# Kernel tuning notes

Hardware: AMD Instinct MI355X
Metric: run time of the kernel (lower is better)

Reference implementation:

```python
import jax, jax.numpy as jnp
import numpy as np

E = 1024
H = 16
HD = E // H  # head_dim = 64
N, T, S = 2, 2048, 2048
NEG = -1e9


def setup_inputs() -> dict:
    key = jax.random.key(0)
    ks = jax.random.split(key, 12)
    s = 0.02
    inp = {
        "query": jax.random.normal(ks[0], (N, T, E), jnp.float32),
        "key": jax.random.normal(ks[1], (N, S, E), jnp.float32),
        "value": jax.random.normal(ks[2], (N, S, E), jnp.float32),
        # causal mask: mask[i, j] == 0 means target i cannot attend to source j
        "attn_mask": jnp.tril(jnp.ones((T, S), jnp.float32)),
        "pad_mask": jnp.zeros((N, S), bool),
        "Wq": jax.random.normal(ks[3], (E, E), jnp.float32) * s,
        "bq": jnp.zeros((E,), jnp.float32),
        "Wk": jax.random.normal(ks[4], (E, E), jnp.float32) * s,
        "bk": jnp.zeros((E,), jnp.float32),
        "Wv": jax.random.normal(ks[5], (E, E), jnp.float32) * s,
        "bv": jnp.zeros((E,), jnp.float32),
        "Wp": jax.random.normal(ks[6], (E, E), jnp.float32) * s,
        "bp": jnp.zeros((E,), jnp.float32),
    }
    return inp


def reference(query, key, value, attn_mask, pad_mask, Wq, bq, Wk, bk, Wv, bv, Wp, bp):
    n, t, _ = query.shape
    _, srcl, _ = key.shape
    # Linear projections (torch Linear: x @ W.T + b), split into heads
    Q = (query @ Wq.T + bq).reshape(n, t, H, HD).transpose(0, 2, 1, 3)      # (N,H,T,HD)
    K = (key @ Wk.T + bk).reshape(n, srcl, H, HD).transpose(0, 2, 1, 3)     # (N,H,S,HD)
    V = (value @ Wv.T + bv).reshape(n, srcl, H, HD).transpose(0, 2, 1, 3)   # (N,H,S,HD)
    scores = jnp.einsum("nhtd,nhsd->nhts", Q, K) / jnp.sqrt(jnp.float32(HD))
    scores = jnp.where(pad_mask[:, None, None, :], NEG, scores)
    scores = jnp.where(attn_mask[None, None, :, :] == 0, NEG, scores)
    att = jax.nn.softmax(scores, axis=-1)  # dropout=0 (eval)
    Y = jnp.einsum("nhts,nhsd->nhtd", att, V)
    Y = Y.transpose(0, 2, 1, 3).reshape(n, t, E)
    return Y @ Wp.T + bp
```

## Files before the change

kernel.cpp:

```cpp
#include <hip/hip_runtime.h>
#include <hip/hip_bf16.h>

#define E_  1024
#define H_  16
#define HD_ 64
#define NB  2
#define T_  2048
#define S_  2048
#define KD  1024

#define QSCALE 0.18033688011112042f

typedef __attribute__((ext_vector_type(8))) short short8;
typedef __attribute__((ext_vector_type(4))) short short4v;
typedef __attribute__((ext_vector_type(4))) float floatx4;

static __device__ __forceinline__ unsigned short f2bf(float f) {
    unsigned int u = __float_as_uint(f);
    unsigned int r = (u + 0x7FFFu + ((u >> 16) & 1u)) >> 16;
    return (unsigned short)r;
}

static __device__ __forceinline__ unsigned short f2bf_fast(float f) {
    return (unsigned short)((__float_as_uint(f) + 0x8000u) >> 16);
}

static __device__ __forceinline__ floatx4 mfma16(short8 a, short8 b, floatx4 c) {
    return __builtin_amdgcn_mfma_f32_16x16x32_bf16(a, b, c, 0, 0, 0);
}

static __device__ __forceinline__ void gload_lds16(const void* g, void* l) {
    __builtin_amdgcn_global_load_lds(
        (const __attribute__((address_space(1))) unsigned int*)g,
        (__attribute__((address_space(3))) unsigned int*)l, 16, 0, 0);
}

#define VMCNT0_BARRIER() do {                                   \
    __builtin_amdgcn_sched_barrier(0);                          \
    asm volatile("s_waitcnt vmcnt(0)" ::: "memory");            \
    __builtin_amdgcn_s_barrier();                               \
    __builtin_amdgcn_sched_barrier(0);                          \
} while (0)

__global__ __launch_bounds__(256) void conv_all_kernel(
    const float* __restrict__ wq, const float* __restrict__ wk,
    const float* __restrict__ wv, const float* __restrict__ wp,
    const float* __restrict__ qi, const float* __restrict__ ki,
    const float* __restrict__ vi,
    unsigned short* __restrict__ Wb, unsigned short* __restrict__ Xb)
{
    const int NW4 = 1 << 18;
    const int NX4 = 1 << 20;
    const int TOT = 4 * NW4 + 3 * NX4;
    int idx = blockIdx.x * 256 + threadIdx.x;
    for (int i4 = idx; i4 < TOT; i4 += 262144) {
        const float* s; unsigned short* d; int off4;
        float sc = 1.0f;
        if (i4 < 4 * NW4) {
            int seg = i4 >> 18; off4 = i4 & (NW4 - 1);
            s = (seg == 0) ? wq : (seg == 1) ? wk : (seg == 2) ? wv : wp;
            d = Wb + ((size_t)seg << 20);
            if (seg == 0) sc = QSCALE;
        } else {
            int j = i4 - 4 * NW4; int seg = j >> 20; off4 = j & (NX4 - 1);
            s = (seg == 0) ? qi : (seg == 1) ? ki : vi;
            d = Xb + ((size_t)seg << 22);
        }
        float4 v = *(const float4*)&s[(size_t)off4 * 4];
        short4v b;
        b[0] = (short)f2bf(v.x * sc); b[1] = (short)f2bf(v.y * sc);
        b[2] = (short)f2bf(v.z * sc); b[3] = (short)f2bf(v.w * sc);
        *(short4v*)&d[(size_t)off4 * 4] = b;
    }
}

__global__ __launch_bounds__(256) void proj_qkv_kernel(
    const unsigned short* __restrict__ Xb, const unsigned short* __restrict__ Wb,
    const float* __restrict__ bq, const float* __restrict__ bk, const float* __restrict__ bv,
    unsigned short* __restrict__ Qh, unsigned short* __restrict__ K2, unsigned short* __restrict__ V2)
{
    const int z = blockIdx.z;
    const unsigned short* X = Xb + ((size_t)z << 22);
    const unsigned short* W = Wb + ((size_t)z << 20);
    const float* bias = (z == 0) ? bq : (z == 1) ? bk : bv;
    unsigned short* dst = (z == 0) ? Qh : (z == 1) ? K2 : V2;

    __shared__ unsigned short Sm[32768];

    const int tid  = threadIdx.x;
    const int lane = tid & 63;
    const int w    = tid >> 6;
    const int wm   = w >> 1, wn = w & 1;
    const int m0   = blockIdx.x * 128;
    const int e0   = blockIdx.y * 128;
    const int l15  = lane & 15, lg = lane >> 4;

    floatx4 acc[4][4];
#pragma unroll
    for (int mi = 0; mi < 4; ++mi)
#pragma unroll
        for (int ni = 0; ni < 4; ++ni)
            acc[mi][ni] = (floatx4){0.f, 0.f, 0.f, 0.f};

    const int rc = lane >> 3;
    const int sl = (lane & 7) ^ rc;

#pragma unroll
    for (int jj = 0; jj < 4; ++jj) {
        int c = w * 4 + jj;
        int row = c * 8 + rc;
        gload_lds16(&X[(size_t)(m0 + row) * KD + sl * 8], &Sm[c * 512]);
        gload_lds16(&W[(size_t)(e0 + row) * KD + sl * 8], &Sm[16384 + c * 512]);
    }
    VMCNT0_BARRIER();

    for (int kt = 0; kt < 16; ++kt) {
        const int cur = (kt & 1) * 8192;
        const int nxt = ((kt + 1) & 1) * 8192;
        const unsigned short* Ac = Sm + cur;
        const unsigned short* Bc = Sm + 16384 + cur;
        unsigned short* An = Sm + nxt;
        unsigned short* Bn = Sm + 16384 + nxt;
        const int k0n = (kt + 1) * 64;

        if (kt < 15) {
#pragma unroll
            for (int jj = 0; jj < 4; ++jj) {
                int c = w * 4 + jj;
                int row = c * 8 + rc;
                gload_lds16(&X[(size_t)(m0 + row) * KD + k0n + sl * 8], &An[c * 512]);
            }
        }
        {
            short8 af[4], bf[4];
#pragma unroll
            for (int mi = 0; mi < 4; ++mi) {
                int r_ = wm * 64 + mi * 16 + l15;
                af[mi] = *(const short8*)&Ac[r_ * 64 + ((lg ^ (r_ & 7)) << 3)];
            }
#pragma unroll
            for (int ni = 0; ni < 4; ++ni) {
                int r_ = wn * 64 + ni * 16 + l15;
                bf[ni] = *(const short8*)&Bc[r_ * 64 + ((lg ^ (r_ & 7)) << 3)];
            }
#pragma unroll
            for (int mi = 0; mi < 4; ++mi)
#pragma unroll
                for (int ni = 0; ni < 4; ++ni)
                    acc[mi][ni] = mfma16(af[mi], bf[ni], acc[mi][ni]);
        }
        if (kt < 15) {
#pragma unroll
            for (int jj = 0; jj < 4; ++jj) {
                int c = w * 4 + jj;
                int row = c * 8 + rc;
                gload_lds16(&W[(size_t)(e0 + row) * KD + k0n + sl * 8], &Bn[c * 512]);
            }
        }
        {
            short8 af[4], bf[4];
#pragma unroll
            for (int mi = 0; mi < 4; ++mi) {
                int r_ = wm * 64 + mi * 16 + l15;
                af[mi] = *(const short8*)&Ac[r_ * 64 + (((4 + lg) ^ (r_ & 7)) << 3)];
            }
#pragma unroll
            for (int ni = 0; ni < 4; ++ni) {
                int r_ = wn * 64 + ni * 16 + l15;
                bf[ni] = *(const short8*)&Bc[r_ * 64 + (((4 + lg) ^ (r_ & 7)) << 3)];
            }
#pragma unroll
            for (int mi = 0; mi < 4; ++mi)
#pragma unroll
                for (int ni = 0; ni < 4; ++ni)
                    acc[mi][ni] = mfma16(af[mi], bf[ni], acc[mi][ni]);
        }
        VMCNT0_BARRIER();
    }

    if (z != 2) {
#pragma unroll
        for (int mi = 0; mi < 4; ++mi)
#pragma unroll
            for (int ni = 0; ni < 4; ++ni) {
                int col = wn * 64 + ni * 16 + l15;
                float bb = bias[e0 + col];
                if (z == 0) bb *= QSCALE;
#pragma unroll
                for (int r = 0; r < 4; ++r) {
                    int row = wm * 64 + mi * 16 + (lg << 2) + r;
                    Sm[row * 128 + (col ^ ((row & 7) << 3))] =
                        f2bf(acc[mi][ni][r] + bb);
                }
            }
    } else {
#pragma unroll
        for (int mi = 0; mi < 4; ++mi)
#pragma unroll
            for (int ni = 0; ni < 4; ++ni) {
                int col = wn * 64 + ni * 16 + l15;
                float bb = bias[e0 + col];
                int rb = wm * 64 + mi * 16 + (lg << 2);
                short4v sv;
#pragma unroll
                for (int r = 0; r < 4; ++r) sv[r] = (short)f2bf(acc[mi][ni][r] + bb);
                *(short4v*)&Sm[col * 128 + (rb ^ ((col & 7) << 3))] = sv;
            }
    }
    __syncthreads();

    {
        const int r0 = tid >> 1;
        const int cb = (tid & 1) * 64;
#pragma unroll
        for (int j = 0; j < 8; ++j) {
            int c = cb + j * 8;
            short8 v = *(const short8*)&Sm[r0 * 128 + (c ^ ((r0 & 7) << 3))];
            if (z == 0) {
                int m = m0 + r0, nn = m >> 11, t = m & (T_ - 1);
                int e = e0 + c, hh = e >> 6, d = e & 63;
                size_t hb = (size_t)(nn * H_ + hh) * (T_ * HD_);
                *(short8*)&dst[hb + (size_t)t * HD_ + d] = v;
            } else if (z == 1) {
                int m = m0 + r0, nn = m >> 11, t = m & (T_ - 1);
                int e = e0 + c, hh = e >> 6, d = e & 63;
                size_t hb = (size_t)(nn * H_ + hh) * (T_ * HD_);
                *(short8*)&dst[hb + (t >> 6) * 4096 + (t & 63) * 64 +
                               (((d >> 3) ^ (t & 7)) << 3)] = v;
            } else {
                int e = e0 + r0, hh = e >> 6, d = e & 63;
                int m = m0 + c, nn = m >> 11, t = m & (T_ - 1);
                size_t hb = (size_t)(nn * H_ + hh) * (T_ * HD_);
                *(short8*)&dst[hb + (t >> 6) * 4096 + d * 64 +
                               ((((t >> 3) & 7) ^ (d & 7)) << 3)] = v;
            }
        }
    }
}

__global__ __launch_bounds__(256) void flash_attn_kernel(
    const unsigned short* __restrict__ Qh, const unsigned short* __restrict__ K2,
    const unsigned short* __restrict__ V2, unsigned short* __restrict__ Y)
{
    const int linear = blockIdx.x;
    const int nid = (linear & 7) * 64 + (linear >> 3);
    const int pb = nid & 15, h = (nid >> 4) & 15, n = nid >> 8;

    const int tid = threadIdx.x, lane = tid & 63, w = tid >> 6;
    const int l15 = lane & 15, lg = lane >> 4;

    const unsigned short* Qp = Qh + (size_t)(n * H_ + h) * (T_ * HD_);
    const unsigned short* Kt = K2 + (size_t)(n * H_ + h) * (T_ * HD_);
    const unsigned short* Vt = V2 + (size_t)(n * H_ + h) * (T_ * HD_);

    __shared__ unsigned short Ks_l[8192];
    __shared__ unsigned short VT_l[8192];
    __shared__ unsigned short Ps[64][136];

    const int prow = w * 16 + lg * 4;
    const int arow = w * 16 + l15;
    const int sw7  = l15 & 7;

#pragma unroll
    for (int side = 0; side < 2; ++side) {
        const int qt = side ? (31 - pb) : pb;
        const int q0 = qt * 64;
        const int nkv = (qt + 2) >> 1;

        short8 qf[2];
#pragma unroll
        for (int ks = 0; ks < 2; ++ks)
            qf[ks] = *(const short8*)&Qp[(size_t)(q0 + arow) * HD_ + ks * 32 + lg * 8];

        floatx4 o[4];
        float lacc[4];
#pragma unroll
        for (int hi = 0; hi < 4; ++hi) o[hi] = (floatx4){0.f, 0.f, 0.f, 0.f};
#pragma unroll
        for (int r = 0; r < 4; ++r) lacc[r] = 0.f;

        for (int kb2 = 0; kb2 < nkv; ++kb2) {
            __syncthreads();
            const unsigned short* Ksrc = Kt + kb2 * 8192;
            const unsigned short* Vsrc = Vt + kb2 * 8192;
#pragma unroll
            for (int j = 0; j < 4; ++j) {
                int c = w * 4 + j;
                gload_lds16(&Ksrc[c * 512 + lane * 8], &Ks_l[c * 512]);
                gload_lds16(&Vsrc[c * 512 + lane * 8], &VT_l[c * 512]);
            }
            __syncthreads();

            floatx4 sa[8];
#pragma unroll
            for (int ni = 0; ni < 8; ++ni) sa[ni] = (floatx4){0.f, 0.f, 0.f, 0.f};
            __builtin_amdgcn_s_setprio(1);
#pragma unroll
            for (int ks = 0; ks < 2; ++ks) {
                short8 kf[8];
#pragma unroll
                for (int ni = 0; ni < 8; ++ni)
                    kf[ni] = *(const short8*)
                        &Ks_l[(ni * 16 + l15) * 64 + (((ks * 4 + lg) ^ sw7) << 3)];
#pragma unroll
                for (int ni = 0; ni < 8; ++ni)
                    sa[ni] = mfma16(qf[ks], kf[ni], sa[ni]);
            }
            __builtin_amdgcn_s_setprio(0);

            const bool diag = (kb2 == nkv - 1);
            const int sbase = kb2 * 128;
            float pv[8][4];
#pragma unroll
            for (int ni = 0; ni < 8; ++ni)
#pragma unroll
                for (int r = 0; r < 4; ++r) {
                    float e = exp2f(sa[ni][r]);
                    if (diag && (sbase + ni * 16 + l15 > q0 + prow + r)) e = 0.f;
                    pv[ni][r] = e;
                }
#pragma unroll
            for (int r = 0; r < 4; ++r)
                lacc[r] += ((pv[0][r] + pv[1][r]) + (pv[2][r] + pv[3][r]))
                         + ((pv[4][r] + pv[5][r]) + (pv[6][r] + pv[7][r]));

#pragma unroll
            for (int ni = 0; ni < 8; ++ni)
#pragma unroll
                for (int r = 0; r < 4; ++r)
                    Ps[prow + r][(ni * 16 + l15) ^ (lg << 3)] = f2bf_fast(pv[ni][r]);

            __builtin_amdgcn_s_setprio(1);
#pragma unroll
            for (int ksp = 0; ksp < 4; ++ksp) {
                short8 pa = *(const short8*)
                    &Ps[arow][(ksp * 32 + lg * 8) ^ ((l15 >> 2) << 3)];
                short8 vt[4];
#pragma unroll
                for (int hi = 0; hi < 4; ++hi)
                    vt[hi] = *(const short8*)
                        &VT_l[(ksp >> 1) * 4096 + (hi * 16 + l15) * 64 +
                              ((((ksp & 1) * 4 + lg) ^ sw7) << 3)];
#pragma unroll
                for (int hi = 0; hi < 4; ++hi)
                    o[hi] = mfma16(pa, vt[hi], o[hi]);
            }
            __builtin_amdgcn_s_setprio(0);
        }

        float linv[4];
#pragma unroll
        for (int r = 0; r < 4; ++r) {
            float l = lacc[r];
#pragma unroll
            for (int off = 1; off < 16; off <<= 1)
                l += __shfl_xor(l, off);
            linv[r] = 1.0f / l;
        }

#pragma unroll
        for (int hi = 0; hi < 4; ++hi) {
            int col = hi * 16 + l15;
#pragma unroll
            for (int r = 0; r < 4; ++r) {
                int t = q0 + prow + r;
                Y[((size_t)n * T_ + t) * E_ + h * HD_ + col] =
                    f2bf(o[hi][r] * linv[r]);
            }
        }
    }
}

__global__ __launch_bounds__(256) void proj_out_kernel(
    const unsigned short* __restrict__ Yb, const unsigned short* __restrict__ Wpb,
    const float* __restrict__ bp, float* __restrict__ out)
{
    __shared__ unsigned short Sm[32768];

    const int tid  = threadIdx.x;
    const int lane = tid & 63;
    const int w    = tid >> 6;
    const int wm   = w >> 1, wn = w & 1;
    const int m0   = blockIdx.x * 128;
    const int e0   = blockIdx.y * 128;
    const int l15  = lane & 15, lg = lane >> 4;

    floatx4 acc[4][4];
#pragma unroll
    for (int mi = 0; mi < 4; ++mi)
#pragma unroll
        for (int ni = 0; ni < 4; ++ni)
            acc[mi][ni] = (floatx4){0.f, 0.f, 0.f, 0.f};

    const int rc = lane >> 3;
    const int sl = (lane & 7) ^ rc;

#pragma unroll
    for (int jj = 0; jj < 4; ++jj) {
        int c = w * 4 + jj;
        int row = c * 8 + rc;
        gload_lds16(&Yb[(size_t)(m0 + row) * E_ + sl * 8], &Sm[c * 512]);
        gload_lds16(&Wpb[(size_t)(e0 + row) * E_ + sl * 8], &Sm[16384 + c * 512]);
    }
    VMCNT0_BARRIER();

    for (int kt = 0; kt < 16; ++kt) {
        const int cur = (kt & 1) * 8192;
        const int nxt = ((kt + 1) & 1) * 8192;
        const unsigned short* Ac = Sm + cur;
        const unsigned short* Bc = Sm + 16384 + cur;
        unsigned short* An = Sm + nxt;
        unsigned short* Bn = Sm + 16384 + nxt;
        const int k0n = (kt + 1) * 64;

        if (kt < 15) {
#pragma unroll
            for (int jj = 0; jj < 4; ++jj) {
                int c = w * 4 + jj;
                int row = c * 8 + rc;
                gload_lds16(&Yb[(size_t)(m0 + row) * E_ + k0n + sl * 8], &An[c * 512]);
            }
        }
        {
            short8 af[4], bf[4];
#pragma unroll
            for (int mi = 0; mi < 4; ++mi) {
                int r_ = wm * 64 + mi * 16 + l15;
                af[mi] = *(const short8*)&Ac[r_ * 64 + ((lg ^ (r_ & 7)) << 3)];
            }
#pragma unroll
            for (int ni = 0; ni < 4; ++ni) {
                int r_ = wn * 64 + ni * 16 + l15;
                bf[ni] = *(const short8*)&Bc[r_ * 64 + ((lg ^ (r_ & 7)) << 3)];
            }
#pragma unroll
            for (int mi = 0; mi < 4; ++mi)
#pragma unroll
                for (int ni = 0; ni < 4; ++ni)
                    acc[mi][ni] = mfma16(af[mi], bf[ni], acc[mi][ni]);
        }
        if (kt < 15) {
#pragma unroll
            for (int jj = 0; jj < 4; ++jj) {
                int c = w * 4 + jj;
                int row = c * 8 + rc;
                gload_lds16(&Wpb[(size_t)(e0 + row) * E_ + k0n + sl * 8], &Bn[c * 512]);
            }
        }
        {
            short8 af[4], bf[4];
#pragma unroll
            for (int mi = 0; mi < 4; ++mi) {
                int r_ = wm * 64 + mi * 16 + l15;
                af[mi] = *(const short8*)&Ac[r_ * 64 + (((4 + lg) ^ (r_ & 7)) << 3)];
            }
#pragma unroll
            for (int ni = 0; ni < 4; ++ni) {
                int r_ = wn * 64 + ni * 16 + l15;
                bf[ni] = *(const short8*)&Bc[r_ * 64 + (((4 + lg) ^ (r_ & 7)) << 3)];
            }
#pragma unroll
            for (int mi = 0; mi < 4; ++mi)
#pragma unroll
                for (int ni = 0; ni < 4; ++ni)
                    acc[mi][ni] = mfma16(af[mi], bf[ni], acc[mi][ni]);
        }
        VMCNT0_BARRIER();
    }

#pragma unroll
    for (int mi = 0; mi < 4; ++mi) {
#pragma unroll
        for (int ni = 0; ni < 4; ++ni) {
            int e = e0 + wn * 64 + ni * 16 + l15;
            float bb = bp[e];
#pragma unroll
            for (int r = 0; r < 4; ++r) {
                int m = m0 + wm * 64 + mi * 16 + (lg << 2) + r;
                out[(size_t)m * E_ + e] = acc[mi][ni][r] + bb;
            }
        }
    }
}

extern "C" void kernel_launch(void* const* d_in, const int* in_sizes, int n_in,
                              void* d_out, int out_size, void* d_ws, size_t ws_size,
                              hipStream_t stream) {
    const float* query = (const float*)d_in[0];
    const float* key_  = (const float*)d_in[1];
    const float* value = (const float*)d_in[2];
    const float* Wq = (const float*)d_in[5];
    const float* bq = (const float*)d_in[6];
    const float* Wk = (const float*)d_in[7];
    const float* bk = (const float*)d_in[8];
    const float* Wv = (const float*)d_in[9];
    const float* bv = (const float*)d_in[10];
    const float* Wp = (const float*)d_in[11];
    const float* bp = (const float*)d_in[12];
    float* out = (float*)d_out;

    const size_t P = (size_t)NB * H_ * T_ * HD_;
    unsigned short* Qh  = (unsigned short*)d_ws;
    unsigned short* K2  = Qh + P;
    unsigned short* V2  = K2 + P;
    unsigned short* Wb  = V2 + P;
    unsigned short* Xb  = Wb + (4u << 20);
    unsigned short* Yb  = Xb;
    unsigned short* Wpb = Wb + (3u << 20);

    conv_all_kernel<<<dim3(1024), 256, 0, stream>>>(
        Wq, Wk, Wv, Wp, query, key_, value, Wb, Xb);
    proj_qkv_kernel<<<dim3(32, 8, 3), 256, 0, stream>>>(
        Xb, Wb, bq, bk, bv, Qh, K2, V2);
    flash_attn_kernel<<<dim3(512), 256, 0, stream>>>(Qh, K2, V2, Yb);
    proj_out_kernel<<<dim3(32, 8), 256, 0, stream>>>(Yb, Wpb, bp, out);
}
```

Baseline: 118.6 us.

## Software-pipeline K/V tile loads into LDS across attention iterations

Restructures the attention inner loop so the next K tile is loaded while P·V runs, and the next V tile is loaded while the next QK^T runs. The old load-then-sync at the top of each iteration is replaced by partial vmcnt waits and barriers. It also swaps exp2f for the raw hardware exp2 builtin. The change adds more barriers and relies on careful vmcnt accounting, so a miscount could create a race on the single-buffered LDS tiles.

```diff
diff --git a/kernel.cpp b/kernel.cpp
--- a/kernel.cpp
+++ b/kernel.cpp
@@ -38,6 +38,13 @@
 #define VMCNT0_BARRIER() do {                                   \
     __builtin_amdgcn_sched_barrier(0);                          \
     asm volatile("s_waitcnt vmcnt(0)" ::: "memory");            \
+    __builtin_amdgcn_s_barrier();                               \
+    __builtin_amdgcn_sched_barrier(0);                          \
+} while (0)
+
+#define VMCNT4_BARRIER() do {                                   \
+    __builtin_amdgcn_sched_barrier(0);                          \
+    asm volatile("s_waitcnt vmcnt(4)" ::: "memory");            \
     __builtin_amdgcn_s_barrier();                               \
     __builtin_amdgcn_sched_barrier(0);                          \
 } while (0)
@@ -279,18 +286,20 @@
 #pragma unroll
         for (int r = 0; r < 4; ++r) lacc[r] = 0.f;
 
+        __builtin_amdgcn_s_barrier();
+#pragma unroll
+        for (int j = 0; j < 4; ++j) {
+            int c = w * 4 + j;
+            gload_lds16(&Kt[c * 512 + lane * 8], &Ks_l[c * 512]);
+        }
+#pragma unroll
+        for (int j = 0; j < 4; ++j) {
+            int c = w * 4 + j;
+            gload_lds16(&Vt[c * 512 + lane * 8], &VT_l[c * 512]);
+        }
+        VMCNT4_BARRIER();
+
         for (int kb2 = 0; kb2 < nkv; ++kb2) {
-            __syncthreads();
-            const unsigned short* Ksrc = Kt + kb2 * 8192;
-            const unsigned short* Vsrc = Vt + kb2 * 8192;
-#pragma unroll
-            for (int j = 0; j < 4; ++j) {
-                int c = w * 4 + j;
-                gload_lds16(&Ksrc[c * 512 + lane * 8], &Ks_l[c * 512]);
-                gload_lds16(&Vsrc[c * 512 + lane * 8], &VT_l[c * 512]);
-            }
-            __syncthreads();
-
             floatx4 sa[8];
 #pragma unroll
             for (int ni = 0; ni < 8; ++ni) sa[ni] = (floatx4){0.f, 0.f, 0.f, 0.f};
@@ -315,7 +324,7 @@
             for (int ni = 0; ni < 8; ++ni)
 #pragma unroll
                 for (int r = 0; r < 4; ++r) {
-                    float e = exp2f(sa[ni][r]);
+                    float e = __builtin_amdgcn_exp2f(sa[ni][r]);
                     if (diag && (sbase + ni * 16 + l15 > q0 + prow + r)) e = 0.f;
                     pv[ni][r] = e;
                 }
@@ -329,6 +338,16 @@
 #pragma unroll
                 for (int r = 0; r < 4; ++r)
                     Ps[prow + r][(ni * 16 + l15) ^ (lg << 3)] = f2bf_fast(pv[ni][r]);
+
+            VMCNT0_BARRIER();
+            if (kb2 + 1 < nkv) {
+                const unsigned short* Ksrc = Kt + (kb2 + 1) * 8192;
+#pragma unroll
+                for (int j = 0; j < 4; ++j) {
+                    int c = w * 4 + j;
+                    gload_lds16(&Ksrc[c * 512 + lane * 8], &Ks_l[c * 512]);
+                }
+            }
 
             __builtin_amdgcn_s_setprio(1);
 #pragma unroll
@@ -346,6 +365,17 @@
                     o[hi] = mfma16(pa, vt[hi], o[hi]);
             }
             __builtin_amdgcn_s_setprio(0);
+
+            __builtin_amdgcn_s_barrier();
+            if (kb2 + 1 < nkv) {
+                const unsigned short* Vsrc = Vt + (kb2 + 1) * 8192;
+#pragma unroll
+                for (int j = 0; j < 4; ++j) {
+                    int c = w * 4 + j;
+                    gload_lds16(&Vsrc[c * 512 + lane * 8], &VT_l[c * 512]);
+                }
+            }
+            VMCNT4_BARRIER();
         }
 
         float linv[4];
```

New measurement: 110.8 us. 6.6% less time.
